# Optimization experiments

Hardware: AMD Instinct MI355X
Metric: run time of the kernel (lower is better)

## Reference

```python
import jax, jax.numpy as jnp
import numpy as np

DIM = 384
H = 65536
P = 3
CORR = 2 * 49 * P * P  # 882


def _lin(x, W, b):
    # x: [H, Cin], W: [Cout, Cin], b: [Cout] -> [H, Cout] (1x1 conv == linear over channels)
    return x @ W.T + b


def setup_inputs() -> dict:
    key = jax.random.key(0)
    ks = jax.random.split(key, 20)
    f32 = jnp.float32

    def rn(k, shape, s=0.02):
        return jax.random.normal(k, shape, f32) * s

    return {
        "net": jax.random.normal(ks[0], (1, DIM, H, 1), f32),
        "inp": jax.random.normal(ks[1], (1, DIM, H, 1), f32),
        "corr": jax.random.normal(ks[2], (1, CORR, H, 1), f32),
        "ii": jax.random.normal(ks[3], (1, 1, H, 1), f32),
        "jj": jax.random.normal(ks[4], (1, 1, H, 1), f32),
        "kk": jax.random.normal(ks[5], (1, 1, H, 1), f32),
        # keep_conv: Conv2d(1,1,1,bias=False) with weight zeroed (frozen)
        "kw": jnp.zeros((), f32),
        # corr_conv: Linear(882->384), ReLU, Linear(384->384), ReLU, Linear(384->384)
        "cc_w1": rn(ks[6], (DIM, CORR)), "cc_b1": jnp.zeros((DIM,), f32),
        "cc_w2": rn(ks[7], (DIM, DIM)), "cc_b2": jnp.zeros((DIM,), f32),
        "cc_w3": rn(ks[8], (DIM, DIM)), "cc_b3": jnp.zeros((DIM,), f32),
        # c1 / c2: Linear(384->384), ReLU, Linear(384->384)
        "c1_w1": rn(ks[9], (DIM, DIM)), "c1_b1": jnp.zeros((DIM,), f32),
        "c1_w2": rn(ks[10], (DIM, DIM)), "c1_b2": jnp.zeros((DIM,), f32),
        "c2_w1": rn(ks[11], (DIM, DIM)), "c2_b1": jnp.zeros((DIM,), f32),
        "c2_w2": rn(ks[12], (DIM, DIM)), "c2_b2": jnp.zeros((DIM,), f32),
        # heads: Linear(384->2)
        "d_w": rn(ks[13], (2, DIM)), "d_b": jnp.zeros((2,), f32),
        "w_w": rn(ks[14], (2, DIM)), "w_b": jnp.zeros((2,), f32),
    }


def reference(net, inp, corr, ii, jj, kk, kw,
              cc_w1, cc_b1, cc_w2, cc_b2, cc_w3, cc_b3,
              c1_w1, c1_b1, c1_w2, c1_b2,
              c2_w1, c2_b1, c2_w2, c2_b2,
              d_w, d_b, w_w, w_b):
    # [1,C,H,1] -> [H,C]
    x = net[0, :, :, 0].T
    y = inp[0, :, :, 0].T
    c = corr[0, :, :, 0].T

    # dummy keep_conv path (zero weight, further scaled by 0.0)
    dummy = (ii + jj + kk)[0, 0, :, 0] * kw  # [H]
    x = x + dummy[:, None] * 0.0

    # corr_conv
    cc = _lin(jax.nn.relu(_lin(jax.nn.relu(_lin(c, cc_w1, cc_b1)), cc_w2, cc_b2)), cc_w3, cc_b3)
    x = x + y + cc

    # net = net + c1(net) + c2(net), both branches read the same pre-update net
    b1 = _lin(jax.nn.relu(_lin(x, c1_w1, c1_b1)), c1_w2, c1_b2)
    b2 = _lin(jax.nn.relu(_lin(x, c2_w1, c2_b1)), c2_w2, c2_b2)
    x = x + b1 + b2

    r = jax.nn.relu(x)
    d_out = _lin(r, d_w, d_b)                      # [H,2]
    w_out = jax.nn.sigmoid(_lin(r, w_w, w_b))      # [H,2]

    # back to [1,C,H,1]
    net_out = x.T[None, :, :, None]
    d_out = d_out.T[None, :, :, None]
    w_out = w_out.T[None, :, :, None]
    return (net_out, d_out, w_out)
```

## Files before the change

kernel.cpp:

```cpp
#include <hip/hip_runtime.h>
#include <hip/hip_bf16.h>

#define H 65536
#define DIMC 384

typedef __bf16 bf16x8 __attribute__((ext_vector_type(8)));
typedef float f32x4 __attribute__((ext_vector_type(4)));

__device__ __forceinline__ unsigned short f2bf(float x) {
    return __builtin_bit_cast(unsigned short, __float2bfloat16(x));
}
__device__ __forceinline__ float bf2f(unsigned short u) {
    return __bfloat162float(__builtin_bit_cast(__hip_bfloat16, u));
}

__global__ __launch_bounds__(256) void wconv_k(
    const float* __restrict__ w1, const float* __restrict__ w2, const float* __restrict__ w3,
    const float* __restrict__ c11, const float* __restrict__ c21,
    const float* __restrict__ c12, const float* __restrict__ c22,
    const float* __restrict__ b11, const float* __restrict__ b21,
    const float* __restrict__ b12, const float* __restrict__ b22,
    unsigned short* __restrict__ dst, float* __restrict__ biasf)
{
    int m = blockIdx.y;
    int gid = blockIdx.x * 256 + threadIdx.x;
    if (m == 7) {
        if (gid < 384)       biasf[gid] = b11[gid];
        else if (gid < 768)  biasf[gid] = b21[gid - 384];
        else if (gid < 1152) biasf[gid] = b12[gid - 768] + b22[gid - 768];
        return;
    }
    if (m == 0) {
        if (gid < 344064) {
            int n = gid / 896, k = gid - n * 896;
            dst[gid] = f2bf(k < 882 ? w1[n * 882 + k] : 0.f);
        }
        return;
    }
    if (gid >= 147456) return;
    const float* src; size_t doff; int Kp = 384, koff = 0;
    switch (m) {
        case 1:  src = c12; doff = 933888; Kp = 768; break;
        default: src = nullptr; doff = 0; break;
    }
    if (m == 1)      { src = w2;  doff = 344064;          Kp = 384; koff = 0;   }
    else if (m == 2) { src = w3;  doff = 491520;          Kp = 384; koff = 0;   }
    else if (m == 3) { src = c11; doff = 638976;          Kp = 384; koff = 0;   }
    else if (m == 4) { src = c21; doff = 638976 + 147456; Kp = 384; koff = 0;   }
    else if (m == 5) { src = c12; doff = 933888;          Kp = 768; koff = 0;   }
    else             { src = c22; doff = 933888;          Kp = 768; koff = 384; }
    int n = gid / 384, k = gid - n * 384;
    dst[doff + (size_t)n * Kp + koff + k] = f2bf(src[gid]);
}

__global__ __launch_bounds__(256) void corr_tconv(const float* __restrict__ src,
                                                  unsigned short* __restrict__ dst)
{
    __shared__ float tile[64][65];
    int hb = blockIdx.x * 64;
    int kb = blockIdx.y * 64;
    int t = threadIdx.x;
    int col = t & 63, r4 = t >> 6;
    #pragma unroll
    for (int p = 0; p < 16; ++p) {
        int row = p * 4 + r4;
        int k = kb + row;
        tile[row][col] = (k < 882) ? src[(size_t)k * H + hb + col] : 0.f;
    }
    __syncthreads();
    #pragma unroll
    for (int p = 0; p < 16; ++p) {
        int hrow = p * 4 + r4;
        dst[(size_t)(hb + hrow) * 896 + kb + col] = f2bf(tile[col][hrow]);
    }
}

template<int MODE>
__global__ __launch_bounds__(256) void gemm_k(
    const unsigned short* __restrict__ W,
    const unsigned short* __restrict__ A,
    const float* __restrict__ bias,
    const float* __restrict__ aux0,
    const float* __restrict__ aux1,
    unsigned short* __restrict__ outb,
    float* __restrict__ outf,
    int Kp, int ldo)
{
    __shared__ unsigned short Wt[128 * 64];
    __shared__ unsigned short At[128 * 64];
    const int tid  = threadIdx.x;
    const int lane = tid & 63;
    const int wave = tid >> 6;
    const int quad = lane >> 4;
    const int l15  = lane & 15;
    const int h0 = blockIdx.x * 128;
    const int c0 = blockIdx.y * 128;
    const int cw = (wave & 1) * 64;
    const int hw = (wave >> 1) * 64;

    const unsigned short* Wbase = W + (size_t)c0 * Kp;
    const unsigned short* Abase = A + (size_t)h0 * Kp;

    f32x4 acc[4][4];
    #pragma unroll
    for (int i = 0; i < 4; ++i)
        #pragma unroll
        for (int j = 0; j < 4; ++j)
            acc[i][j] = f32x4{0.f, 0.f, 0.f, 0.f};

    const int srow = tid >> 3;
    const int skc  = (tid & 7) * 8;

    for (int kt = 0; kt < Kp; kt += 64) {
        __syncthreads();
        #pragma unroll
        for (int i = 0; i < 4; ++i) {
            const unsigned short* g = Wbase + (size_t)(i * 32 + srow) * Kp + kt + skc;
            char* lb = (char*)Wt + (i * 256 + wave * 64) * 16;
            __builtin_amdgcn_global_load_lds((__attribute__((address_space(1))) void*)(void*)g,
                                             (__attribute__((address_space(3))) void*)lb, 16, 0, 0);
        }
        #pragma unroll
        for (int i = 0; i < 4; ++i) {
            const unsigned short* g = Abase + (size_t)(i * 32 + srow) * Kp + kt + skc;
            char* lb = (char*)At + (i * 256 + wave * 64) * 16;
            __builtin_amdgcn_global_load_lds((__attribute__((address_space(1))) void*)(void*)g,
                                             (__attribute__((address_space(3))) void*)lb, 16, 0, 0);
        }
        __syncthreads();

        const uint4* Wv = (const uint4*)Wt;
        const uint4* Av = (const uint4*)At;
        #pragma unroll
        for (int ks = 0; ks < 2; ++ks) {
            uint4 aw[4], bx[4];
            #pragma unroll
            for (int ci = 0; ci < 4; ++ci) aw[ci] = Wv[(cw + ci * 16 + l15) * 8 + ks * 4 + quad];
            #pragma unroll
            for (int hi = 0; hi < 4; ++hi) bx[hi] = Av[(hw + hi * 16 + l15) * 8 + ks * 4 + quad];
            #pragma unroll
            for (int ci = 0; ci < 4; ++ci)
                #pragma unroll
                for (int hi = 0; hi < 4; ++hi)
                    acc[ci][hi] = __builtin_amdgcn_mfma_f32_16x16x32_bf16(
                        __builtin_bit_cast(bf16x8, aw[ci]),
                        __builtin_bit_cast(bf16x8, bx[hi]),
                        acc[ci][hi], 0, 0, 0);
        }
    }

    #pragma unroll
    for (int ci = 0; ci < 4; ++ci) {
        const int c = c0 + cw + ci * 16 + quad * 4;
        f32x4 b4 = *(const f32x4*)(bias + c);
        #pragma unroll
        for (int hi = 0; hi < 4; ++hi) {
            const int h = h0 + hw + hi * 16 + l15;
            const size_t base = (size_t)h * ldo + c;
            f32x4 v = acc[ci][hi] + b4;
            if constexpr (MODE == 1) {
                #pragma unroll
                for (int r = 0; r < 4; ++r)
                    v[r] += aux0[(size_t)(c + r) * H + h] + aux1[(size_t)(c + r) * H + h];
                *(f32x4*)(outf + base) = v;
            }
            if constexpr (MODE == 3) {
                v += *(const f32x4*)(aux0 + base);
                #pragma unroll
                for (int r = 0; r < 4; ++r)
                    outf[(size_t)(c + r) * H + h] = v[r];
            }
            f32x4 s = v;
            if constexpr (MODE == 0 || MODE == 3) {
                s[0] = fmaxf(s[0], 0.f); s[1] = fmaxf(s[1], 0.f);
                s[2] = fmaxf(s[2], 0.f); s[3] = fmaxf(s[3], 0.f);
            }
            ushort4 o;
            o.x = f2bf(s[0]); o.y = f2bf(s[1]); o.z = f2bf(s[2]); o.w = f2bf(s[3]);
            *(ushort4*)(outb + base) = o;
        }
    }
}

__global__ __launch_bounds__(256) void heads_k(
    const unsigned short* __restrict__ r,
    const float* __restrict__ dW, const float* __restrict__ dB,
    const float* __restrict__ wW, const float* __restrict__ wB,
    float* __restrict__ out)
{
    __shared__ float wl[1536];
    int tid = threadIdx.x;
    for (int i = tid; i < 1536; i += 256)
        wl[i] = (i < 768) ? dW[i] : wW[i - 768];
    __syncthreads();
    int wave = tid >> 6, lane = tid & 63;
    int h = blockIdx.x * 4 + wave;
    const unsigned short* rp = r + (size_t)h * 384 + lane * 6;
    int c = lane * 6;
    float s0 = 0.f, s1 = 0.f, s2 = 0.f, s3 = 0.f;
    #pragma unroll
    for (int i = 0; i < 6; ++i) {
        float rv = bf2f(rp[i]);
        s0 += rv * wl[c + i];
        s1 += rv * wl[384 + c + i];
        s2 += rv * wl[768 + c + i];
        s3 += rv * wl[1152 + c + i];
    }
    #pragma unroll
    for (int m = 32; m >= 1; m >>= 1) {
        s0 += __shfl_xor(s0, m, 64);
        s1 += __shfl_xor(s1, m, 64);
        s2 += __shfl_xor(s2, m, 64);
        s3 += __shfl_xor(s3, m, 64);
    }
    if (lane == 0) {
        float* od = out + (size_t)384 * H;
        float* ow = out + (size_t)386 * H;
        od[h]     = s0 + dB[0];
        od[H + h] = s1 + dB[1];
        ow[h]     = 1.f / (1.f + __expf(-(s2 + wB[0])));
        ow[H + h] = 1.f / (1.f + __expf(-(s3 + wB[1])));
    }
}

extern "C" void kernel_launch(void* const* d_in, const int* in_sizes, int n_in,
                              void* d_out, int out_size, void* d_ws, size_t ws_size,
                              hipStream_t stream)
{
    const float* net   = (const float*)d_in[0];
    const float* inp   = (const float*)d_in[1];
    const float* corr  = (const float*)d_in[2];
    const float* cc_w1 = (const float*)d_in[7];
    const float* cc_b1 = (const float*)d_in[8];
    const float* cc_w2 = (const float*)d_in[9];
    const float* cc_b2 = (const float*)d_in[10];
    const float* cc_w3 = (const float*)d_in[11];
    const float* cc_b3 = (const float*)d_in[12];
    const float* c1_w1 = (const float*)d_in[13];
    const float* c1_b1 = (const float*)d_in[14];
    const float* c1_w2 = (const float*)d_in[15];
    const float* c1_b2 = (const float*)d_in[16];
    const float* c2_w1 = (const float*)d_in[17];
    const float* c2_b1 = (const float*)d_in[18];
    const float* c2_w2 = (const float*)d_in[19];
    const float* c2_b2 = (const float*)d_in[20];
    const float* d_wp  = (const float*)d_in[21];
    const float* d_bp  = (const float*)d_in[22];
    const float* w_wp  = (const float*)d_in[23];
    const float* w_bp  = (const float*)d_in[24];
    float* out = (float*)d_out;

    char* ws = (char*)d_ws;
    size_t off = 0;
    auto carve = [&](size_t bytes) -> char* {
        char* p = ws + off;
        off += (bytes + 255) & ~(size_t)255;
        return p;
    };
    unsigned short* Wreg  = (unsigned short*)carve((size_t)1228800 * 2);
    unsigned short* corrb = (unsigned short*)carve((size_t)H * 896 * 2);
    unsigned short* t1    = (unsigned short*)carve((size_t)H * 384 * 2);
    unsigned short* t2    = (unsigned short*)carve((size_t)H * 384 * 2);
    float*          xf    = (float*)carve((size_t)H * 384 * 4);
    unsigned short* xb    = (unsigned short*)carve((size_t)H * 384 * 2);
    float*          biasf = (float*)carve((size_t)1152 * 4);

    unsigned short* w1b = Wreg;
    unsigned short* w2b = Wreg + 344064;
    unsigned short* w3b = Wreg + 491520;
    unsigned short* cAb = Wreg + 638976;
    unsigned short* cBb = Wreg + 933888;

    wconv_k<<<dim3(1344, 8), 256, 0, stream>>>(cc_w1, cc_w2, cc_w3, c1_w1, c2_w1, c1_w2, c2_w2,
                                               c1_b1, c2_b1, c1_b2, c2_b2, Wreg, biasf);
    corr_tconv<<<dim3(1024, 14), 256, 0, stream>>>(corr, corrb);

    gemm_k<0><<<dim3(512, 3), 256, 0, stream>>>(w1b, corrb, cc_b1, nullptr, nullptr, t1, nullptr, 896, 384);
    gemm_k<0><<<dim3(512, 3), 256, 0, stream>>>(w2b, t1, cc_b2, nullptr, nullptr, t2, nullptr, 384, 384);
    gemm_k<1><<<dim3(512, 3), 256, 0, stream>>>(w3b, t2, cc_b3, net, inp, xb, xf, 384, 384);
    gemm_k<0><<<dim3(512, 6), 256, 0, stream>>>(cAb, xb, biasf, nullptr, nullptr, corrb, nullptr, 384, 768);
    gemm_k<3><<<dim3(512, 3), 256, 0, stream>>>(cBb, corrb, biasf + 768, xf, nullptr, t1, out, 768, 384);

    heads_k<<<H / 4, 256, 0, stream>>>(t1, d_wp, d_bp, w_wp, w_bp, out);
}
```

Before: 977.6 us.

## Swizzle GEMM LDS tiles and stage transposed epilogue I/O through shared memory

XOR-swizzles the 16-byte chunk index in the LDS staging of both GEMM operand tiles, so the MFMA fragment reads stop hitting the same banks. The MODE 1 epilogue now reads the channel-major aux inputs (net and inp) with coalesced vector loads into LDS and then adds them per fragment. The MODE 3 epilogue writes the channel-major fp32 output through an LDS transpose, replacing the strided scalar global accesses. The cost is extra syncthreads and LDS round trips in the epilogue, and the shared buffer is reused, which depends on correct barrier placement.

```diff
diff --git a/kernel.cpp b/kernel.cpp
--- a/kernel.cpp
+++ b/kernel.cpp
@@ -39,10 +39,6 @@
     }
     if (gid >= 147456) return;
     const float* src; size_t doff; int Kp = 384, koff = 0;
-    switch (m) {
-        case 1:  src = c12; doff = 933888; Kp = 768; break;
-        default: src = nullptr; doff = 0; break;
-    }
     if (m == 1)      { src = w2;  doff = 344064;          Kp = 384; koff = 0;   }
     else if (m == 2) { src = w3;  doff = 491520;          Kp = 384; koff = 0;   }
     else if (m == 3) { src = c11; doff = 638976;          Kp = 384; koff = 0;   }
@@ -86,8 +82,9 @@
     float* __restrict__ outf,
     int Kp, int ldo)
 {
-    __shared__ unsigned short Wt[128 * 64];
-    __shared__ unsigned short At[128 * 64];
+    __shared__ __align__(16) char SMEM[32768];
+    unsigned short* Wt = (unsigned short*)SMEM;
+    unsigned short* At = (unsigned short*)(SMEM + 16384);
     const int tid  = threadIdx.x;
     const int lane = tid & 63;
     const int wave = tid >> 6;
@@ -109,7 +106,8 @@
             acc[i][j] = f32x4{0.f, 0.f, 0.f, 0.f};
 
     const int srow = tid >> 3;
-    const int skc  = (tid & 7) * 8;
+    const int skc  = ((tid & 7) ^ (srow & 7)) * 8;
+    const int rswz = l15 & 7;
 
     for (int kt = 0; kt < Kp; kt += 64) {
         __syncthreads();
@@ -135,9 +133,11 @@
         for (int ks = 0; ks < 2; ++ks) {
             uint4 aw[4], bx[4];
             #pragma unroll
-            for (int ci = 0; ci < 4; ++ci) aw[ci] = Wv[(cw + ci * 16 + l15) * 8 + ks * 4 + quad];
+            for (int ci = 0; ci < 4; ++ci)
+                aw[ci] = Wv[(cw + ci * 16 + l15) * 8 + ((ks * 4 + quad) ^ rswz)];
             #pragma unroll
-            for (int hi = 0; hi < 4; ++hi) bx[hi] = Av[(hw + hi * 16 + l15) * 8 + ks * 4 + quad];
+            for (int hi = 0; hi < 4; ++hi)
+                bx[hi] = Av[(hw + hi * 16 + l15) * 8 + ((ks * 4 + quad) ^ rswz)];
             #pragma unroll
             for (int ci = 0; ci < 4; ++ci)
                 #pragma unroll
@@ -154,21 +154,82 @@
         const int c = c0 + cw + ci * 16 + quad * 4;
         f32x4 b4 = *(const f32x4*)(bias + c);
         #pragma unroll
+        for (int hi = 0; hi < 4; ++hi) acc[ci][hi] += b4;
+    }
+
+    if constexpr (MODE == 1) {
+        float* F = (float*)SMEM;
+        __syncthreads();
+        #pragma unroll
+        for (int hh = 0; hh < 2; ++hh) {
+            #pragma unroll 2
+            for (int p = 0; p < 8; ++p) {
+                int s = p * 256 + tid;
+                int row = s >> 4, c4 = s & 15;
+                size_t gi = (size_t)(c0 + row) * H + h0 + hh * 64 + c4 * 4;
+                f32x4 a = *(const f32x4*)(aux0 + gi);
+                f32x4 b = *(const f32x4*)(aux1 + gi);
+                *(f32x4*)(F + row * 64 + c4 * 4) = a + b;
+            }
+            __syncthreads();
+            if (hw == hh * 64) {
+                #pragma unroll
+                for (int ci = 0; ci < 4; ++ci)
+                    #pragma unroll
+                    for (int hi = 0; hi < 4; ++hi)
+                        #pragma unroll
+                        for (int r = 0; r < 4; ++r)
+                            acc[ci][hi][r] += F[(cw + ci * 16 + quad * 4 + r) * 64 + hi * 16 + l15];
+            }
+            __syncthreads();
+        }
+    }
+
+    if constexpr (MODE == 3) {
+        #pragma unroll
+        for (int ci = 0; ci < 4; ++ci) {
+            const int c = c0 + cw + ci * 16 + quad * 4;
+            #pragma unroll
+            for (int hi = 0; hi < 4; ++hi) {
+                const int h = h0 + hw + hi * 16 + l15;
+                acc[ci][hi] += *(const f32x4*)(aux0 + (size_t)h * ldo + c);
+            }
+        }
+        float* G = (float*)SMEM;
+        __syncthreads();
+        #pragma unroll
+        for (int hh = 0; hh < 2; ++hh) {
+            if (hw == hh * 64) {
+                #pragma unroll
+                for (int ci = 0; ci < 4; ++ci)
+                    #pragma unroll
+                    for (int hi = 0; hi < 4; ++hi)
+                        #pragma unroll
+                        for (int r = 0; r < 4; ++r)
+                            G[(cw + ci * 16 + quad * 4 + r) * 64 + hi * 16 + l15] = acc[ci][hi][r];
+            }
+            __syncthreads();
+            #pragma unroll 2
+            for (int p = 0; p < 8; ++p) {
+                int s = p * 256 + tid;
+                int row = s >> 4, c4 = s & 15;
+                *(f32x4*)(outf + (size_t)(c0 + row) * H + h0 + hh * 64 + c4 * 4) =
+                    *(const f32x4*)(G + row * 64 + c4 * 4);
+            }
+            __syncthreads();
+        }
+    }
+
+    #pragma unroll
+    for (int ci = 0; ci < 4; ++ci) {
+        const int c = c0 + cw + ci * 16 + quad * 4;
+        #pragma unroll
         for (int hi = 0; hi < 4; ++hi) {
             const int h = h0 + hw + hi * 16 + l15;
             const size_t base = (size_t)h * ldo + c;
-            f32x4 v = acc[ci][hi] + b4;
+            f32x4 v = acc[ci][hi];
             if constexpr (MODE == 1) {
-                #pragma unroll
-                for (int r = 0; r < 4; ++r)
-                    v[r] += aux0[(size_t)(c + r) * H + h] + aux1[(size_t)(c + r) * H + h];
                 *(f32x4*)(outf + base) = v;
-            }
-            if constexpr (MODE == 3) {
-                v += *(const f32x4*)(aux0 + base);
-                #pragma unroll
-                for (int r = 0; r < 4; ++r)
-                    outf[(size_t)(c + r) * H + h] = v[r];
             }
             f32x4 s = v;
             if constexpr (MODE == 0 || MODE == 3) {
```

Measured after the change: 947.9 us. 3.0% less time.
